# Kernel tuning notes

Measured on AMD Instinct MI355X. Metric: run time of the kernel, lower is better.

The kernel has to match this reference:

```python
import jax, jax.numpy as jnp
import numpy as np
from jax import lax

NEG_INF = -1e30  # safe log-zero in fp32
EPS = 1e-7       # Keras backend epsilon used inside ctc_batch_cost


def _shift(x, n):
    # shift right along last axis by n, filling with NEG_INF
    return jnp.pad(x[:, :-n], ((0, 0), (n, 0)), constant_values=NEG_INF)


def _lse3(a, b, c):
    m = jnp.maximum(jnp.maximum(a, b), c)
    return m + jnp.log(jnp.exp(a - m) + jnp.exp(b - m) + jnp.exp(c - m))


def ctc_batch_cost(y_true, y_hat):
    # y_true: [B, L] int labels; y_hat: [B, T, C] softmax probabilities.
    # Keras semantics: blank = C-1, input_len = T, label_len = L for every row.
    B, T, C = y_hat.shape
    L = y_true.shape[1]
    S = 2 * L + 1
    blank = C - 1

    logp = jnp.log(y_hat + EPS)  # [B, T, C]

    # extended label sequence: blank, l0, blank, l1, ..., blank  -> [B, S]
    ext = jnp.full((B, S), blank, dtype=jnp.int32).at[:, 1::2].set(y_true.astype(jnp.int32))

    # gather log-probs of extended labels: [B, T, S] -> time-major [T, B, S]
    lp = jnp.take_along_axis(logp, ext[:, None, :], axis=2)
    lp = jnp.transpose(lp, (1, 0, 2))

    # skip-transition allowed at s if ext[s] != blank and ext[s] != ext[s-2]
    pos = jnp.arange(S)
    skip = (pos >= 2) & (ext != blank) & (ext != jnp.roll(ext, 2, axis=1))  # [B, S]

    alpha0 = jnp.full((B, S), NEG_INF, dtype=logp.dtype)
    alpha0 = alpha0.at[:, 0].set(lp[0, :, 0]).at[:, 1].set(lp[0, :, 1])

    def step(alpha, lp_t):
        a1 = _shift(alpha, 1)
        a2 = jnp.where(skip, _shift(alpha, 2), NEG_INF)
        alpha_new = lp_t + _lse3(alpha, a1, a2)
        return alpha_new, None

    alpha, _ = lax.scan(step, alpha0, lp[1:])  # final alpha: [B, S]

    loss = -jnp.logaddexp(alpha[:, S - 1], alpha[:, S - 2])  # [B]
    return loss[:, None]  # [B, 1], matching K.ctc_batch_cost


def setup_inputs() -> dict:
    key = jax.random.key(0)
    k1, k2 = jax.random.split(key)
    B, T, C, L = 64, 1024, 512, 128
    logits = jax.random.normal(k1, (B, T, C), dtype=jnp.float32)
    y_hat = jax.nn.softmax(logits, axis=-1)  # module consumes softmax probs
    y_true = jax.random.randint(k2, (B, L), 0, C - 1, dtype=jnp.int32)  # avoid blank=C-1
    return {"y_true": y_true, "y_hat": y_hat}


def reference(y_true, y_hat):
    return ctc_batch_cost(y_true, y_hat)
```

## Files before the change

### kernel.cpp

```cpp
#include <hip/hip_runtime.h>


constexpr int   B_DIM = 64;
constexpr int   T_LEN = 1024;
constexpr int   C_DIM = 512;
constexpr int   L_LEN = 128;
constexpr int   BLANK = C_DIM - 1;
constexpr int   HALF  = T_LEN / 2;
constexpr int   TC    = 16;
constexpr int   NCH   = HALF / TC;
constexpr int   NBUF  = 4;
constexpr float EPSF  = 1e-7f;
constexpr float LN2F  = 0.69314718055994530942f;

__device__ __forceinline__ float wshr1_f(float x) {
    return __int_as_float(__builtin_amdgcn_update_dpp(
        0, __float_as_int(x), 0x138, 0xf, 0xf, true));
}
__device__ __forceinline__ int wshr1_i(int x) {
    return __builtin_amdgcn_update_dpp(0, x, 0x138, 0xf, 0xf, true);
}
__device__ __forceinline__ float wshl1_f(float x) {
    return __int_as_float(__builtin_amdgcn_update_dpp(
        0, __float_as_int(x), 0x130, 0xf, 0xf, true));
}
__device__ __forceinline__ int wshl1_i(int x) {
    return __builtin_amdgcn_update_dpp(0, x, 0x130, 0xf, 0xf, true);
}

__global__ __launch_bounds__(128, 1)
void ctc_fb(const int* __restrict__ yt, const float* __restrict__ yh,
            float* __restrict__ st)
{
    __shared__ float sbuf[NBUF][TC][C_DIM];

    const int bid  = blockIdx.x;
    const int b    = bid >> 1;
    const int dir  = bid & 1;
    const int tid  = threadIdx.x;
    const int lane = tid & 63;
    const int wid  = tid >> 6;

    const int* __restrict__ lb = yt + b * L_LEN;
    const float* __restrict__ yhb = yh + (size_t)b * T_LEN * C_DIM;

    if (wid == 1) {
        auto stage = [&](int ch) {
            float* d = &sbuf[ch & (NBUF - 1)][0][0];
            const int row0 = dir == 0 ? ch * TC : T_LEN - TC * (ch + 1);
            const float* g = yhb + (size_t)row0 * C_DIM + lane * 4;
#pragma unroll
            for (int i = 0; i < TC; ++i) {
#pragma unroll
                for (int h = 0; h < 2; ++h) {
                    __builtin_amdgcn_global_load_lds(
                        (const __attribute__((address_space(1))) void*)
                            (g + i * C_DIM + h * 256),
                        (__attribute__((address_space(3))) void*)
                            (d + i * C_DIM + h * 256),
                        16, 0, 0);
                }
            }
        };
        asm volatile("s_waitcnt vmcnt(0)" ::: "memory");
        stage(0);
        stage(1);
        asm volatile("s_waitcnt vmcnt(32)" ::: "memory");
        __builtin_amdgcn_sched_barrier(0);
        __builtin_amdgcn_s_barrier();
#pragma unroll 1
        for (int c = 0; c < NCH; ++c) {
            if (c + 2 < NCH) {
                stage(c + 2);
                asm volatile("s_waitcnt vmcnt(32)" ::: "memory");
            } else {
                asm volatile("s_waitcnt vmcnt(0)" ::: "memory");
            }
            __builtin_amdgcn_sched_barrier(0);
            __builtin_amdgcn_s_barrier();
        }
        return;
    }

    const int l0 = lb[2 * lane];
    const int l1 = lb[2 * lane + 1];
    float* me = st + ((size_t)(dir * B_DIM + b) * 64 + lane) * 6;

    if (dir == 0) {
        const int lp = lane ? lb[2 * lane - 1] : 0;
        const float sk1 = (lane > 0 && l0 != lp && l0 != BLANK) ? 1.0f : 0.0f;
        const float sk3 = (l1 != l0 && l1 != BLANK) ? 1.0f : 0.0f;

        float a0 = (lane == 0) ? 1.0f : 0.0f;
        float a1 = 0.0f, a2 = 0.0f, a3 = 0.0f, a4 = 0.0f;
        int   E  = 0;
        float sSeed = (lane == 0) ? 0.0f : 1.0f;

        __builtin_amdgcn_s_barrier();

        float r1[8], r3[8], rb[8];
#pragma unroll 1
        for (int c = 0; c < NCH; ++c) {
            __builtin_amdgcn_sched_barrier(0);
            const float* sb = &sbuf[c & (NBUF - 1)][0][0];
#pragma unroll
            for (int i = 0; i < 8; ++i) {
                r1[i] = sb[i * C_DIM + l0];
                r3[i] = sb[i * C_DIM + l1];
                rb[i] = sb[i * C_DIM + BLANK];
            }
#pragma unroll
            for (int tq = 0; tq < 2; ++tq) {
#pragma unroll
                for (int i = 0; i < 8; ++i) {
                    const float P1 = r1[i] + EPSF;
                    const float P3 = r3[i] + EPSF;
                    const float Pb = rb[i] + EPSF;
                    if (tq == 0) {
                        r1[i] = sb[(i + 8) * C_DIM + l0];
                        r3[i] = sb[(i + 8) * C_DIM + l1];
                        rb[i] = sb[(i + 8) * C_DIM + BLANK];
                    }
                    const float pa3 = wshr1_f(a3) * sSeed;
                    const float n0 = Pb * (a0 + pa3);
                    const float n1 = P1 * (a1 + a0 + sk1 * pa3);
                    const float n2 = Pb * (a2 + a1);
                    const float n3 = P3 * (a3 + a2 + sk3 * a1);
                    const float n4 = Pb * (a4 + a3);
                    a0 = n0; a1 = n1; a2 = n2; a3 = n3; a4 = n4;

                    if ((i & 3) == 3) {
                        const float m = fmaxf(fmaxf(fmaxf(a0, a1), fmaxf(a2, a3)), a4);
                        const bool has = m > 0.0f;
                        int eb = (int)((__float_as_uint(m) >> 23) & 0xFFu);
                        eb = eb < 1 ? 1 : eb;
                        if (has) {
                            const float scl = __uint_as_float((unsigned)(254 - eb) << 23);
                            a0 *= scl; a1 *= scl; a2 *= scl; a3 *= scl; a4 *= scl;
                            E += eb - 127;
                        }
                        int pE = wshr1_i(E);
                        if (!has && lane > 0) E = pE;
                        pE = wshr1_i(E);
                        const int d = pE - E;
                        sSeed = (lane == 0 || d < -126)
                              ? 0.0f
                              : __uint_as_float((unsigned)(127 + (d > 126 ? 126 : d)) << 23);
                    }
                }
            }
            __builtin_amdgcn_sched_barrier(0);
            __builtin_amdgcn_s_barrier();
        }
        me[0] = a0; me[1] = a1; me[2] = a2; me[3] = a3; me[4] = a4;
        me[5] = __int_as_float(E);
    } else {
        const float skb1 = (l1 != l0 && l1 != BLANK) ? 1.0f : 0.0f;
        const int ln = (lane < 63) ? lb[2 * lane + 2] : 0;
        const float skb3 = (lane < 63 && ln != l1 && ln != BLANK) ? 1.0f : 0.0f;

        float c0 = 0.0f, c1 = 0.0f, c2 = 0.0f;
        float c3 = (lane == 63) ? 1.0f : 0.0f;
        float c4 = (lane == 63) ? 1.0f : 0.0f;
        int   E  = 0;
        float sSeed = (lane == 63) ? 0.0f : 1.0f;

        __builtin_amdgcn_s_barrier();

        float r1[8], r3[8], rb[8];
#pragma unroll 1
        for (int c = 0; c < NCH; ++c) {
            __builtin_amdgcn_sched_barrier(0);
            const float* sb = &sbuf[c & (NBUF - 1)][0][0];
#pragma unroll
            for (int i = 0; i < 8; ++i) {
                const int rr = TC - 1 - i;
                r1[i] = sb[rr * C_DIM + l0];
                r3[i] = sb[rr * C_DIM + l1];
                rb[i] = sb[rr * C_DIM + BLANK];
            }
#pragma unroll
            for (int tq = 0; tq < 2; ++tq) {
#pragma unroll
                for (int i = 0; i < 8; ++i) {
                    const float P1 = r1[i] + EPSF;
                    const float P3 = r3[i] + EPSF;
                    const float Pb = rb[i] + EPSF;
                    if (tq == 0) {
                        const int rr = 7 - i;
                        r1[i] = sb[rr * C_DIM + l0];
                        r3[i] = sb[rr * C_DIM + l1];
                        rb[i] = sb[rr * C_DIM + BLANK];
                    }
                    const float bn0 = c0 * Pb;
                    const float bn1 = c1 * P1;
                    const float bn2 = c2 * Pb;
                    const float bn3 = c3 * P3;
                    const float bn4 = c4 * Pb;
                    const float x1  = wshl1_f(bn1) * sSeed;
                    c0 = bn0 + bn1;
                    c1 = bn1 + bn2 + skb1 * bn3;
                    c2 = bn2 + bn3;
                    c3 = bn3 + bn4 + skb3 * x1;
                    c4 = bn4 + x1;

                    if ((i & 3) == 3) {
                        const float m = fmaxf(fmaxf(fmaxf(c0, c1), fmaxf(c2, c3)), c4);
                        const bool has = m > 0.0f;
                        int eb = (int)((__float_as_uint(m) >> 23) & 0xFFu);
                        eb = eb < 1 ? 1 : eb;
                        if (has) {
                            const float scl = __uint_as_float((unsigned)(254 - eb) << 23);
                            c0 *= scl; c1 *= scl; c2 *= scl; c3 *= scl; c4 *= scl;
                            E += eb - 127;
                        }
                        int pE = wshl1_i(E);
                        if (!has && lane < 63) E = pE;
                        pE = wshl1_i(E);
                        const int d = pE - E;
                        sSeed = (lane == 63 || d < -126)
                              ? 0.0f
                              : __uint_as_float((unsigned)(127 + (d > 126 ? 126 : d)) << 23);
                    }
                }
            }
            __builtin_amdgcn_sched_barrier(0);
            __builtin_amdgcn_s_barrier();
        }
        me[0] = c0; me[1] = c1; me[2] = c2; me[3] = c3; me[4] = c4;
        me[5] = __int_as_float(E);
    }
}

__global__ __launch_bounds__(64)
void ctc_combine(const float* __restrict__ st, float* __restrict__ out)
{
    const int b    = blockIdx.x;
    const int lane = threadIdx.x;
    const float* f = st + ((size_t)b * 64 + lane) * 6;
    const float* g = st + ((size_t)(B_DIM + b) * 64 + lane) * 6;

    float v = f[0] * g[0] + f[1] * g[1] + f[2] * g[2] + f[3] * g[3];
    if (lane == 63) v += f[4] * g[4];
    const int e = __float_as_int(f[5]) + __float_as_int(g[5]);
    float L = (v > 0.0f) ? (log2f(v) + (float)e) : -1e30f;

    float M = L;
#pragma unroll
    for (int d = 1; d < 64; d <<= 1) M = fmaxf(M, __shfl_xor(M, d));
    float s = (L > -1e29f) ? exp2f(L - M) : 0.0f;
#pragma unroll
    for (int d = 1; d < 64; d <<= 1) s += __shfl_xor(s, d);

    if (lane == 0) out[b] = -((M + log2f(s)) * LN2F);
}

extern "C" void kernel_launch(void* const* d_in, const int* in_sizes, int n_in,
                              void* d_out, int out_size, void* d_ws, size_t ws_size,
                              hipStream_t stream)
{
    const int*   yt  = (const int*)d_in[0];
    const float* yh  = (const float*)d_in[1];
    float*       out = (float*)d_out;
    float*       st  = (float*)d_ws;
    ctc_fb<<<dim3(2 * B_DIM), dim3(128), 0, stream>>>(yt, yh, st);
    ctc_combine<<<dim3(B_DIM), dim3(64), 0, stream>>>(st, out);
}
```

Measured before the change: 41.08 us.

## Move label-probability gathers into producer wave via compacted LDS staging

The producer wave now gathers each chunk's label and blank probabilities, with epsilon already added, from the staged rows into a compact per-lane float2 array plus a broadcast blank array. The consumer wave then reads contiguous, conflict-free values instead of doing scattered row gathers inside its serial recurrence. Row buffering drops from four buffers to two, and the producer must finish each gather one chunk ahead. This takes LDS latency and the epsilon adds off the critical dependency chain, but it adds producer work and LDS traffic, and the two-buffer scheme has less slack.

```diff
diff --git a/kernel.cpp b/kernel.cpp
--- a/kernel.cpp
+++ b/kernel.cpp
@@ -9,7 +9,6 @@
 constexpr int   HALF  = T_LEN / 2;
 constexpr int   TC    = 16;
 constexpr int   NCH   = HALF / TC;
-constexpr int   NBUF  = 4;
 constexpr float EPSF  = 1e-7f;
 constexpr float LN2F  = 0.69314718055994530942f;
 
@@ -32,7 +31,9 @@
 void ctc_fb(const int* __restrict__ yt, const float* __restrict__ yh,
             float* __restrict__ st)
 {
-    __shared__ float sbuf[NBUF][TC][C_DIM];
+    __shared__ float  rowbuf[2][TC][C_DIM];
+    __shared__ float2 cmp[2][TC][64];
+    __shared__ float  blk[2][TC];
 
     const int bid  = blockIdx.x;
     const int b    = bid >> 1;
@@ -44,9 +45,12 @@
     const int* __restrict__ lb = yt + b * L_LEN;
     const float* __restrict__ yhb = yh + (size_t)b * T_LEN * C_DIM;
 
+    const int l0 = lb[2 * lane];
+    const int l1 = lb[2 * lane + 1];
+
     if (wid == 1) {
-        auto stage = [&](int ch) {
-            float* d = &sbuf[ch & (NBUF - 1)][0][0];
+        auto stageRows = [&](int ch) {
+            float* d = &rowbuf[ch & 1][0][0];
             const int row0 = dir == 0 ? ch * TC : T_LEN - TC * (ch + 1);
             const float* g = yhb + (size_t)row0 * C_DIM + lane * 4;
 #pragma unroll
@@ -62,28 +66,43 @@
                 }
             }
         };
+        auto gatherCmp = [&](int ch) {
+            const float* r = &rowbuf[ch & 1][0][0];
+#pragma unroll
+            for (int i = 0; i < TC; ++i) {
+                const int rr = dir == 0 ? i : TC - 1 - i;
+                const float v1 = r[rr * C_DIM + l0];
+                const float v3 = r[rr * C_DIM + l1];
+                const float vb = r[rr * C_DIM + BLANK];
+                cmp[ch & 1][i][lane] = make_float2(v1 + EPSF, v3 + EPSF);
+                if (lane == 0) blk[ch & 1][i] = vb + EPSF;
+            }
+        };
+
         asm volatile("s_waitcnt vmcnt(0)" ::: "memory");
-        stage(0);
-        stage(1);
+        stageRows(0);
+        stageRows(1);
         asm volatile("s_waitcnt vmcnt(32)" ::: "memory");
+        gatherCmp(0);
+        asm volatile("s_waitcnt lgkmcnt(0)" ::: "memory");
         __builtin_amdgcn_sched_barrier(0);
         __builtin_amdgcn_s_barrier();
 #pragma unroll 1
         for (int c = 0; c < NCH; ++c) {
             if (c + 2 < NCH) {
-                stage(c + 2);
+                stageRows(c + 2);
                 asm volatile("s_waitcnt vmcnt(32)" ::: "memory");
             } else {
                 asm volatile("s_waitcnt vmcnt(0)" ::: "memory");
             }
+            if (c + 1 < NCH) gatherCmp(c + 1);
+            asm volatile("s_waitcnt lgkmcnt(0)" ::: "memory");
             __builtin_amdgcn_sched_barrier(0);
             __builtin_amdgcn_s_barrier();
         }
         return;
     }
 
-    const int l0 = lb[2 * lane];
-    const int l1 = lb[2 * lane + 1];
     float* me = st + ((size_t)(dir * B_DIM + b) * 64 + lane) * 6;
 
     if (dir == 0) {
@@ -98,29 +117,23 @@
 
         __builtin_amdgcn_s_barrier();
 
-        float r1[8], r3[8], rb[8];
+        float2 r13[8]; float rbk[8];
 #pragma unroll 1
         for (int c = 0; c < NCH; ++c) {
             __builtin_amdgcn_sched_barrier(0);
-            const float* sb = &sbuf[c & (NBUF - 1)][0][0];
-#pragma unroll
-            for (int i = 0; i < 8; ++i) {
-                r1[i] = sb[i * C_DIM + l0];
-                r3[i] = sb[i * C_DIM + l1];
-                rb[i] = sb[i * C_DIM + BLANK];
-            }
+            const float2* cp = &cmp[c & 1][0][0];
+            const float*  bp = &blk[c & 1][0];
+#pragma unroll
+            for (int i = 0; i < 8; ++i) { r13[i] = cp[i * 64 + lane]; rbk[i] = bp[i]; }
 #pragma unroll
             for (int tq = 0; tq < 2; ++tq) {
 #pragma unroll
                 for (int i = 0; i < 8; ++i) {
-                    const float P1 = r1[i] + EPSF;
-                    const float P3 = r3[i] + EPSF;
-                    const float Pb = rb[i] + EPSF;
-                    if (tq == 0) {
-                        r1[i] = sb[(i + 8) * C_DIM + l0];
-                        r3[i] = sb[(i + 8) * C_DIM + l1];
-                        rb[i] = sb[(i + 8) * C_DIM + BLANK];
-                    }
+                    const float P1 = r13[i].x;
+                    const float P3 = r13[i].y;
+                    const float Pb = rbk[i];
+                    if (tq == 0) { r13[i] = cp[(i + 8) * 64 + lane]; rbk[i] = bp[i + 8]; }
+
                     const float pa3 = wshr1_f(a3) * sSeed;
                     const float n0 = Pb * (a0 + pa3);
                     const float n1 = P1 * (a1 + a0 + sk1 * pa3);
@@ -167,31 +180,23 @@
 
         __builtin_amdgcn_s_barrier();
 
-        float r1[8], r3[8], rb[8];
+        float2 r13[8]; float rbk[8];
 #pragma unroll 1
         for (int c = 0; c < NCH; ++c) {
             __builtin_amdgcn_sched_barrier(0);
-            const float* sb = &sbuf[c & (NBUF - 1)][0][0];
-#pragma unroll
-            for (int i = 0; i < 8; ++i) {
-                const int rr = TC - 1 - i;
-                r1[i] = sb[rr * C_DIM + l0];
-                r3[i] = sb[rr * C_DIM + l1];
-                rb[i] = sb[rr * C_DIM + BLANK];
-            }
+            const float2* cp = &cmp[c & 1][0][0];
+            const float*  bp = &blk[c & 1][0];
+#pragma unroll
+            for (int i = 0; i < 8; ++i) { r13[i] = cp[i * 64 + lane]; rbk[i] = bp[i]; }
 #pragma unroll
             for (int tq = 0; tq < 2; ++tq) {
 #pragma unroll
                 for (int i = 0; i < 8; ++i) {
-                    const float P1 = r1[i] + EPSF;
-                    const float P3 = r3[i] + EPSF;
-                    const float Pb = rb[i] + EPSF;
-                    if (tq == 0) {
-                        const int rr = 7 - i;
-                        r1[i] = sb[rr * C_DIM + l0];
-                        r3[i] = sb[rr * C_DIM + l1];
-                        rb[i] = sb[rr * C_DIM + BLANK];
-                    }
+                    const float P1 = r13[i].x;
+                    const float P3 = r13[i].y;
+                    const float Pb = rbk[i];
+                    if (tq == 0) { r13[i] = cp[(i + 8) * 64 + lane]; rbk[i] = bp[i + 8]; }
+
                     const float bn0 = c0 * Pb;
                     const float bn1 = c1 * P1;
                     const float bn2 = c2 * Pb;
```

New measurement: 76.76 us. 1.87x slower.
